# Optimization experiments

Measured on AMD Instinct MI355X. Metric: run time of the kernel, lower is better.

## Reference

```python
import jax, jax.numpy as jnp
import numpy as np

LN_EPS = 1e-5
NORM_EPS = 1e-12  # F.normalize eps


def _l2norm(x):
    # torch F.normalize(p=2, dim=-1): x / max(||x||, eps)
    n = jnp.sqrt(jnp.sum(x * x, axis=-1, keepdims=True))
    return x / jnp.maximum(n, NORM_EPS)


def setup_inputs() -> dict:
    key = jax.random.key(0)
    D, R, H = 256, 32, 64  # d_model, rank, d_model//4
    B, C, P = 32, 64, 96
    ks = jax.random.split(key, 16)
    s = 0.05
    return {
        "x": jax.random.normal(ks[0], (B * C, P, D), jnp.float32),
        "ln_gamma": jnp.ones((D,), jnp.float32),
        "ln_beta": jnp.zeros((D,), jnp.float32),
        "Wd": jax.random.normal(ks[1], (D, R), jnp.float32) * s,
        "bd": jax.random.normal(ks[2], (R,), jnp.float32) * s,
        "Wq": jax.random.normal(ks[3], (R, R), jnp.float32) * s,
        "Wk": jax.random.normal(ks[4], (R, R), jnp.float32) * s,
        "Wv": jax.random.normal(ks[5], (R, R), jnp.float32) * s,
        "Wg": jax.random.normal(ks[6], (R, R), jnp.float32) * s,
        "bg": jax.random.normal(ks[7], (R,), jnp.float32) * s,
        "Wu": jax.random.normal(ks[8], (R, D), jnp.float32) * s,
        "bu": jax.random.normal(ks[9], (D,), jnp.float32) * s,
        "W1": jax.random.normal(ks[10], (D, H), jnp.float32) * s,
        "b1": jax.random.normal(ks[11], (H,), jnp.float32) * s,
        "W2": jax.random.normal(ks[12], (H, D), jnp.float32) * s,
        "b2": jnp.full((D,), -5.0, jnp.float32),  # gate_init bias
        "B": B,
        "C": C,
    }


def reference(x, ln_gamma, ln_beta, Wd, bd, Wq, Wk, Wv, Wg, bg, Wu, bu, W1, b1, W2, b2, B, C):
    BC, P, D = x.shape
    # [B*C, P, D] -> [B*P, C, D] channel-mixing layout
    h = x.reshape(B, C, P, D).transpose(0, 2, 1, 3).reshape(B * P, C, D)

    # LayerNorm over D (biased variance, as in torch LayerNorm)
    mu = jnp.mean(h, axis=-1, keepdims=True)
    var = jnp.var(h, axis=-1, keepdims=True)
    h_norm = (h - mu) * jax.lax.rsqrt(var + LN_EPS) * ln_gamma + ln_beta

    # bottleneck projection to rank R
    h_low = h_norm @ Wd + bd  # [BP, C, R]

    # Hydra linear attention: cosine-normalized Q/K, sum-pooled K*V global feature
    Q = _l2norm(h_low @ Wq)
    K = _l2norm(h_low @ Wk)
    V = h_low @ Wv
    global_feat = jnp.sum(K * V, axis=1, keepdims=True)  # [BP, 1, R]
    h_attn = Q * global_feat

    # content gate and up-projection
    gate_c = jax.nn.sigmoid(h_low @ Wg + bg)
    mixed = (h_attn * gate_c) @ Wu + bu  # [BP, C, D]

    # AdaptiveGate: unbiased variance over channel dim (torch .var default ddof=1)
    chan_var = jnp.var(h, axis=1, ddof=1)  # [BP, D]
    gate_logits = jax.nn.gelu(chan_var @ W1 + b1, approximate=False) @ W2 + b2
    gate = jax.nn.sigmoid(gate_logits)[:, None, :]  # [BP, 1, D]

    out = h + gate * mixed
    # back to [B*C, P, D]
    return out.reshape(B, P, C, D).transpose(0, 2, 1, 3).reshape(BC, P, D)
```

## Files before the change

kernel.cpp:

```cpp
#include <hip/hip_runtime.h>

#define DD 256
#define RR 32
#define CC 64
#define PB 96
#define NT 1024

typedef __attribute__((ext_vector_type(8))) short short8;
typedef __attribute__((ext_vector_type(4))) float f32x4;

__device__ __forceinline__ unsigned short f2b(float f) {
    union { float f; unsigned u; } v; v.f = f;
    unsigned r = v.u + 0x7fffu + ((v.u >> 16) & 1u);
    return (unsigned short)(r >> 16);
}
__device__ __forceinline__ float b2f(unsigned short s) {
    union { unsigned u; float f; } v; v.u = ((unsigned)s) << 16;
    return v.f;
}

__device__ __forceinline__ int hidx(int c, int d) {
    return c * 256 + ((((d >> 3) ^ (c & 7)) << 3) | (d & 7));
}
__device__ __forceinline__ int nidx(int row, int k) {
    return row * 32 + ((((k >> 3) ^ ((row >> 1) & 3)) << 3) | (k & 7));
}

__global__ __launch_bounds__(NT, 8)
void hydra_kernel(const float* __restrict__ x,
                  const float* __restrict__ ln_g, const float* __restrict__ ln_b,
                  const float* __restrict__ Wd, const float* __restrict__ bd,
                  const float* __restrict__ Wq, const float* __restrict__ Wk,
                  const float* __restrict__ Wv, const float* __restrict__ Wg,
                  const float* __restrict__ bg,
                  const float* __restrict__ Wu, const float* __restrict__ bu,
                  const float* __restrict__ W1, const float* __restrict__ b1,
                  const float* __restrict__ W2, const float* __restrict__ b2,
                  float* __restrict__ out)
{
    __shared__ short hbf[CC * DD];
    __shared__ short wreg[RR * DD];
    __shared__ short lowbuf[CC * RR];
    __shared__ short qgkv[2 * CC * RR];
    __shared__ float redA[2048];
    __shared__ float redB[2048];
    __shared__ float mu_s[CC], rstd_s[CC];
    __shared__ float cv_s[DD], gate_s[DD];
    __shared__ float hid_s[64];
    __shared__ float ln_a[RR], ln_bv[RR];

    const int t    = threadIdx.x;
    const int lane = t & 63;
    const int w    = t >> 6;
    const int bp   = blockIdx.x;
    const int b    = bp / PB;
    const int p    = bp - b * PB;
    const size_t rowbase = (size_t)(b * CC) * PB * DD + (size_t)p * DD;

    #pragma unroll
    for (int i = 0; i < 4; ++i) {
        const int c = w * 4 + i;
        const float4 v = *(const float4*)(x + rowbase + (size_t)c * (PB * DD) + 4 * lane);
        float s1 = v.x + v.y + v.z + v.w;
        float s2 = v.x * v.x + v.y * v.y + v.z * v.z + v.w * v.w;
        #pragma unroll
        for (int off = 32; off; off >>= 1) {
            s1 += __shfl_xor(s1, off, 64);
            s2 += __shfl_xor(s2, off, 64);
        }
        if (lane == 0) {
            const float mu = s1 * (1.f / 256.f);
            mu_s[c]   = mu;
            rstd_s[c] = rsqrtf(s2 * (1.f / 256.f) - mu * mu + 1e-5f);
        }
        ushort4 pk;
        pk.x = f2b(v.x); pk.y = f2b(v.y); pk.z = f2b(v.z); pk.w = f2b(v.w);
        *(ushort4*)&hbf[hidx(c, 4 * lane)] = pk;
    }
    {
        const int r = t >> 5, dblk = t & 31;
        short8 vv;
        float sa = 0.f, sb = 0.f;
        #pragma unroll
        for (int j = 0; j < 8; ++j) {
            const int d = dblk * 8 + j;
            const float wd = Wd[d * RR + r];
            const float g  = ln_g[d];
            vv[j] = (short)f2b(g * wd);
            sa += g * wd;
            sb += ln_b[d] * wd;
        }
        *(short8*)&wreg[r * 256 + ((dblk ^ (r & 7)) << 3)] = vv;
        redA[r * 32 + dblk]        = sa;
        redA[1024 + r * 32 + dblk] = sb;
    }
    __syncthreads();

    f32x4 s3acc = {0.f, 0.f, 0.f, 0.f};
    if (w < 8) {
        const int ct = w >> 1, rt = w & 1;
        const int arow = ct * 16 + (lane & 15);
        const int brow = rt * 16 + (lane & 15);
        const int ksub = lane >> 4;
        #pragma unroll
        for (int step = 0; step < 8; ++step) {
            const int kb = step * 4 + ksub;
            const short8 a  = *(const short8*)&hbf[arow * 256 + ((kb ^ (arow & 7)) << 3)];
            const short8 bf = *(const short8*)&wreg[brow * 256 + ((kb ^ (brow & 7)) << 3)];
            s3acc = __builtin_amdgcn_mfma_f32_16x16x32_bf16(a, bf, s3acc, 0, 0, 0);
        }
    } else {
        const int idx = t - 512;
        const int dp  = idx & 127;
        const int rg  = idx >> 7;
        const int d0  = dp * 2;
        float s1a = 0.f, s1b = 0.f, s2a = 0.f, s2b = 0.f;
        #pragma unroll 4
        for (int i = 0; i < 16; ++i) {
            const int c = rg * 16 + i;
            const ushort2 u = *(const ushort2*)&hbf[hidx(c, d0)];
            const float va = b2f(u.x), vb = b2f(u.y);
            s1a += va; s2a += va * va;
            s1b += vb; s2b += vb * vb;
        }
        *(float2*)&redB[rg * 256 + d0]        = make_float2(s1a, s1b);
        *(float2*)&redB[1024 + rg * 256 + d0] = make_float2(s2a, s2b);
        if (idx < 64) {
            const int r = idx & 31, which = idx >> 5;
            float s = 0.f;
            for (int g = 0; g < 32; ++g) s += redA[which * 1024 + r * 32 + g];
            if (which == 0) ln_a[r] = s;
            else            ln_bv[r] = s + bd[r];
        }
    }
    __syncthreads();

    if (w < 8) {
        const int ct = w >> 1, rt = w & 1;
        const int col = rt * 16 + (lane & 15);
        const float la = ln_a[col], lb = ln_bv[col];
        #pragma unroll
        for (int i = 0; i < 4; ++i) {
            const int c = ct * 16 + (lane >> 4) * 4 + i;
            const float rs = rstd_s[c];
            const float hl = rs * s3acc[i] - rs * mu_s[c] * la + lb;
            lowbuf[nidx(c, col)] = (short)f2b(hl);
        }
    } else {
        const int slot = t - 512;
        const int m = slot >> 7, rr2 = (slot >> 2) & 31, kg = slot & 3;
        const float* Wm = (m == 0) ? Wq : (m == 1) ? Wk : (m == 2) ? Wv : Wg;
        short8 vv;
        #pragma unroll
        for (int j = 0; j < 8; ++j)
            vv[j] = (short)f2b(Wm[(kg * 8 + j) * RR + rr2]);
        *(short8*)&wreg[m * 1024 + nidx(rr2, kg * 8)] = vv;
    }
    if (t < 256) {
        const float S1 = redB[t] + redB[256 + t] + redB[512 + t] + redB[768 + t];
        const float S2 = redB[1024 + t] + redB[1280 + t] + redB[1536 + t] + redB[1792 + t];
        cv_s[t] = (S2 - S1 * S1 * (1.f / 64.f)) * (1.f / 63.f);
    }
    __syncthreads();

    if (w < 8) {
        const int ct = w >> 1, pair = w & 1;
        const int mA = pair ? 1 : 0;
        const int mB = pair ? 2 : 3;
        const int arow = ct * 16 + (lane & 15);
        const int ksub = lane >> 4;
        const short8 a = *(const short8*)&lowbuf[arow * 32 + ((ksub ^ ((arow >> 1) & 3)) << 3)];
        f32x4 aA0 = {0,0,0,0}, aA1 = {0,0,0,0}, aB0 = {0,0,0,0}, aB1 = {0,0,0,0};
        {
            const int br0 = (lane & 15), br1 = 16 + (lane & 15);
            const short8 bA0 = *(const short8*)&wreg[mA * 1024 + br0 * 32 + ((ksub ^ ((br0 >> 1) & 3)) << 3)];
            const short8 bA1 = *(const short8*)&wreg[mA * 1024 + br1 * 32 + ((ksub ^ ((br1 >> 1) & 3)) << 3)];
            const short8 bB0 = *(const short8*)&wreg[mB * 1024 + br0 * 32 + ((ksub ^ ((br0 >> 1) & 3)) << 3)];
            const short8 bB1 = *(const short8*)&wreg[mB * 1024 + br1 * 32 + ((ksub ^ ((br1 >> 1) & 3)) << 3)];
            aA0 = __builtin_amdgcn_mfma_f32_16x16x32_bf16(a, bA0, aA0, 0, 0, 0);
            aA1 = __builtin_amdgcn_mfma_f32_16x16x32_bf16(a, bA1, aA1, 0, 0, 0);
            aB0 = __builtin_amdgcn_mfma_f32_16x16x32_bf16(a, bB0, aB0, 0, 0, 0);
            aB1 = __builtin_amdgcn_mfma_f32_16x16x32_bf16(a, bB1, aB1, 0, 0, 0);
        }
        float qs[4];
        #pragma unroll
        for (int i = 0; i < 4; ++i) {
            float ss = aA0[i] * aA0[i] + aA1[i] * aA1[i];
            ss += __shfl_xor(ss, 1, 64);
            ss += __shfl_xor(ss, 2, 64);
            ss += __shfl_xor(ss, 4, 64);
            ss += __shfl_xor(ss, 8, 64);
            qs[i] = 1.f / fmaxf(sqrtf(ss), 1e-12f);
        }
        const int col0 = (lane & 15), col1 = 16 + (lane & 15);
        float bgv0 = 0.f, bgv1 = 0.f;
        if (pair == 0) { bgv0 = bg[col0]; bgv1 = bg[col1]; }
        #pragma unroll
        for (int i = 0; i < 4; ++i) {
            const int c = ct * 16 + (lane >> 4) * 4 + i;
            float b0 = aB0[i], b1v = aB1[i];
            if (pair == 0) {
                b0  = 1.f / (1.f + __expf(-(b0 + bgv0)));
                b1v = 1.f / (1.f + __expf(-(b1v + bgv1)));
            }
            qgkv[pair * 2048 + c * 32 + col0] = (short)f2b(aA0[i] * qs[i] * b0);
            qgkv[pair * 2048 + c * 32 + col1] = (short)f2b(aA1[i] * qs[i] * b1v);
        }
    } else {
        const int idx = t - 512;
        const int j = idx & 63, dg = idx >> 6;
        float s = 0.f;
        #pragma unroll 8
        for (int i = 0; i < 32; ++i) {
            const int d = dg * 32 + i;
            s += cv_s[d] * W1[d * 64 + j];
        }
        redA[dg * 64 + j] = s;
    }
    __syncthreads();

    if (t < 64) {
        float s = b1[t];
        #pragma unroll
        for (int g = 0; g < 8; ++g) s += redA[g * 64 + t];
        hid_s[t] = 0.5f * s * (1.f + erff(s * 0.70710678118654752f));
    }
    if (t >= 256 && t < 512) {
        const int idx = t - 256;
        const int r = idx & 31, g = idx >> 5;
        float s = 0.f;
        #pragma unroll
        for (int i = 0; i < 8; ++i)
            s += b2f((unsigned short)qgkv[2048 + (g * 8 + i) * 32 + r]);
        redA[512 + g * 32 + r] = s;
    }
    {
        const int d = t & 255, kg = t >> 8;
        short8 vv;
        #pragma unroll
        for (int j = 0; j < 8; ++j)
            vv[j] = (short)f2b(Wu[(kg * 8 + j) * DD + d]);
        *(short8*)&wreg[nidx(d, kg * 8)] = vv;
    }
    __syncthreads();

    {
        const int d = t & 255, jg = t >> 8;
        float s = 0.f;
        #pragma unroll
        for (int i = 0; i < 16; ++i) {
            const int j = jg * 16 + i;
            s += hid_s[j] * W2[j * DD + d];
        }
        redB[jg * 256 + d] = s;
    }
    {
        const int r = t & 31, c0 = t >> 5, c1 = (t >> 5) + 32;
        float gf = 0.f;
        #pragma unroll
        for (int g = 0; g < 8; ++g) gf += redA[512 + g * 32 + r];
        lowbuf[nidx(c0, r)] = (short)f2b(b2f((unsigned short)qgkv[c0 * 32 + r]) * gf);
        lowbuf[nidx(c1, r)] = (short)f2b(b2f((unsigned short)qgkv[c1 * 32 + r]) * gf);
    }
    __syncthreads();

    {
        const int ct = w & 3, dg = w >> 2;
        const int arow = ct * 16 + (lane & 15);
        const int ksub = lane >> 4;
        const short8 a = *(const short8*)&lowbuf[arow * 32 + ((ksub ^ ((arow >> 1) & 3)) << 3)];
        #pragma unroll
        for (int j = 0; j < 4; ++j) {
            const int dt = dg * 4 + j;
            const int col = dt * 16 + (lane & 15);
            const short8 bf = *(const short8*)&wreg[col * 32 + ((ksub ^ ((col >> 1) & 3)) << 3)];
            f32x4 acc = {0.f, 0.f, 0.f, 0.f};
            acc = __builtin_amdgcn_mfma_f32_16x16x32_bf16(a, bf, acc, 0, 0, 0);
            #pragma unroll
            for (int i = 0; i < 4; ++i) {
                const int c = ct * 16 + (lane >> 4) * 4 + i;
                hbf[hidx(c, col)] = (short)f2b(acc[i]);
            }
        }
    }
    if (t < 256) {
        const float s = redB[t] + redB[256 + t] + redB[512 + t] + redB[768 + t] + b2[t];
        gate_s[t] = 1.f / (1.f + __expf(-s));
    }
    __syncthreads();

    #pragma unroll
    for (int i = 0; i < 4; ++i) {
        const int c = w * 4 + i;
        const size_t off = rowbase + (size_t)c * (PB * DD) + 4 * lane;
        const float4 xv = *(const float4*)(x + off);
        const ushort4 m = *(const ushort4*)&hbf[hidx(c, 4 * lane)];
        const float4 g4 = *(const float4*)&gate_s[4 * lane];
        const float4 bu4 = *(const float4*)(bu + 4 * lane);
        float4 o;
        o.x = xv.x + g4.x * (b2f(m.x) + bu4.x);
        o.y = xv.y + g4.y * (b2f(m.y) + bu4.y);
        o.z = xv.z + g4.z * (b2f(m.z) + bu4.z);
        o.w = xv.w + g4.w * (b2f(m.w) + bu4.w);
        *(float4*)(out + off) = o;
    }
}

extern "C" void kernel_launch(void* const* d_in, const int* in_sizes, int n_in,
                              void* d_out, int out_size, void* d_ws, size_t ws_size,
                              hipStream_t stream) {
    (void)in_sizes; (void)n_in; (void)out_size; (void)d_ws; (void)ws_size;
    const float* x    = (const float*)d_in[0];
    const float* ln_g = (const float*)d_in[1];
    const float* ln_b = (const float*)d_in[2];
    const float* Wd   = (const float*)d_in[3];
    const float* bd   = (const float*)d_in[4];
    const float* Wq   = (const float*)d_in[5];
    const float* Wk   = (const float*)d_in[6];
    const float* Wv   = (const float*)d_in[7];
    const float* Wg   = (const float*)d_in[8];
    const float* bg   = (const float*)d_in[9];
    const float* Wu   = (const float*)d_in[10];
    const float* bu   = (const float*)d_in[11];
    const float* W1   = (const float*)d_in[12];
    const float* b1   = (const float*)d_in[13];
    const float* W2   = (const float*)d_in[14];
    const float* b2   = (const float*)d_in[15];
    float* out = (float*)d_out;

    hydra_kernel<<<dim3(32 * PB), dim3(NT), 0, stream>>>(
        x, ln_g, ln_b, Wd, bd, Wq, Wk, Wv, Wg, bg, Wu, bu, W1, b1, W2, b2, out);
}
```

Baseline: 166.2 us.

## Precompute bf16 swizzled weights in a prep kernel and shrink shared memory

```diff
diff --git a/kernel.cpp b/kernel.cpp
--- a/kernel.cpp
+++ b/kernel.cpp
@@ -26,23 +26,81 @@
     return row * 32 + ((((k >> 3) ^ ((row >> 1) & 3)) << 3) | (k & 7));
 }
 
+__global__ __launch_bounds__(1024, 1)
+void prep_kernel(const float* __restrict__ ln_g, const float* __restrict__ ln_b,
+                 const float* __restrict__ Wd, const float* __restrict__ bd,
+                 const float* __restrict__ Wq, const float* __restrict__ Wk,
+                 const float* __restrict__ Wv, const float* __restrict__ Wg,
+                 const float* __restrict__ Wu,
+                 short* __restrict__ wsWd, short* __restrict__ wsQKVG,
+                 short* __restrict__ wsWu, float* __restrict__ wsLN)
+{
+    __shared__ float redp[2048];
+    const int t = threadIdx.x;
+    {
+        const int r = t >> 5, dblk = t & 31;
+        short8 vv;
+        float sa = 0.f, sb = 0.f;
+        #pragma unroll
+        for (int j = 0; j < 8; ++j) {
+            const int d = dblk * 8 + j;
+            const float wd = Wd[d * RR + r];
+            const float g  = ln_g[d];
+            vv[j] = (short)f2b(g * wd);
+            sa += g * wd;
+            sb += ln_b[d] * wd;
+        }
+        *(short8*)&wsWd[r * 256 + ((dblk ^ (r & 7)) << 3)] = vv;
+        redp[r * 32 + dblk]        = sa;
+        redp[1024 + r * 32 + dblk] = sb;
+    }
+    if (t < 512) {
+        const int m = t >> 7, rr2 = (t >> 2) & 31, kg = t & 3;
+        const float* Wm = (m == 0) ? Wq : (m == 1) ? Wk : (m == 2) ? Wv : Wg;
+        short8 vv;
+        #pragma unroll
+        for (int j = 0; j < 8; ++j)
+            vv[j] = (short)f2b(Wm[(kg * 8 + j) * RR + rr2]);
+        *(short8*)&wsQKVG[m * 1024 + rr2 * 32 + ((kg ^ ((rr2 >> 1) & 3)) << 3)] = vv;
+    }
+    {
+        const int d = t & 255, kg = t >> 8;
+        short8 vv;
+        #pragma unroll
+        for (int j = 0; j < 8; ++j)
+            vv[j] = (short)f2b(Wu[(kg * 8 + j) * DD + d]);
+        *(short8*)&wsWu[d * 32 + ((kg ^ ((d >> 1) & 3)) << 3)] = vv;
+    }
+    __syncthreads();
+    if (t < 32) {
+        float s = 0.f;
+        #pragma unroll
+        for (int g = 0; g < 32; ++g) s += redp[t * 32 + g];
+        wsLN[t] = s;
+    } else if (t < 64) {
+        const int r = t - 32;
+        float s = 0.f;
+        #pragma unroll
+        for (int g = 0; g < 32; ++g) s += redp[1024 + r * 32 + g];
+        wsLN[t] = s + bd[r];
+    }
+}
+
 __global__ __launch_bounds__(NT, 8)
 void hydra_kernel(const float* __restrict__ x,
-                  const float* __restrict__ ln_g, const float* __restrict__ ln_b,
-                  const float* __restrict__ Wd, const float* __restrict__ bd,
-                  const float* __restrict__ Wq, const float* __restrict__ Wk,
-                  const float* __restrict__ Wv, const float* __restrict__ Wg,
+                  const short* __restrict__ wsWd, const short* __restrict__ wsQKVG,
+                  const short* __restrict__ wsWu, const float* __restrict__ wsLN,
                   const float* __restrict__ bg,
-                  const float* __restrict__ Wu, const float* __restrict__ bu,
+                  const float* __restrict__ bu,
                   const float* __restrict__ W1, const float* __restrict__ b1,
                   const float* __restrict__ W2, const float* __restrict__ b2,
                   float* __restrict__ out)
 {
     __shared__ short hbf[CC * DD];
-    __shared__ short wreg[RR * DD];
+    __shared__ short wreg[RR * DD / 2];
+    __shared__ short qg[CC * RR];
     __shared__ short lowbuf[CC * RR];
-    __shared__ short qgkv[2 * CC * RR];
-    __shared__ float redA[2048];
+    __shared__ float redA[1024];
     __shared__ float redB[2048];
     __shared__ float mu_s[CC], rstd_s[CC];
     __shared__ float cv_s[DD], gate_s[DD];
@@ -77,23 +135,9 @@
         pk.x = f2b(v.x); pk.y = f2b(v.y); pk.z = f2b(v.z); pk.w = f2b(v.w);
         *(ushort4*)&hbf[hidx(c, 4 * lane)] = pk;
     }
-    {
-        const int r = t >> 5, dblk = t & 31;
-        short8 vv;
-        float sa = 0.f, sb = 0.f;
-        #pragma unroll
-        for (int j = 0; j < 8; ++j) {
-            const int d = dblk * 8 + j;
-            const float wd = Wd[d * RR + r];
-            const float g  = ln_g[d];
-            vv[j] = (short)f2b(g * wd);
-            sa += g * wd;
-            sb += ln_b[d] * wd;
-        }
-        *(short8*)&wreg[r * 256 + ((dblk ^ (r & 7)) << 3)] = vv;
-        redA[r * 32 + dblk]        = sa;
-        redA[1024 + r * 32 + dblk] = sb;
-    }
+    *(short8*)&wreg[t * 8] = *(const short8*)&wsWd[t * 8];
+    if (t < 32)              ln_a[t]       = wsLN[t];
+    else if (t < 64)         ln_bv[t - 32] = wsLN[t];
     __syncthreads();
 
     f32x4 s3acc = {0.f, 0.f, 0.f, 0.f};
@@ -125,13 +169,6 @@
         }
         *(float2*)&redB[rg * 256 + d0]        = make_float2(s1a, s1b);
         *(float2*)&redB[1024 + rg * 256 + d0] = make_float2(s2a, s2b);
-        if (idx < 64) {
-            const int r = idx & 31, which = idx >> 5;
-            float s = 0.f;
-            for (int g = 0; g < 32; ++g) s += redA[which * 1024 + r * 32 + g];
-            if (which == 0) ln_a[r] = s;
-            else            ln_bv[r] = s + bd[r];
-        }
     }
     __syncthreads();
 
@@ -147,14 +184,8 @@
             lowbuf[nidx(c, col)] = (short)f2b(hl);
         }
     } else {
-        const int slot = t - 512;
-        const int m = slot >> 7, rr2 = (slot >> 2) & 31, kg = slot & 3;
-        const float* Wm = (m == 0) ? Wq : (m == 1) ? Wk : (m == 2) ? Wv : Wg;
-        short8 vv;
-        #pragma unroll
-        for (int j = 0; j < 8; ++j)
-            vv[j] = (short)f2b(Wm[(kg * 8 + j) * RR + rr2]);
-        *(short8*)&wreg[m * 1024 + nidx(rr2, kg * 8)] = vv;
+        const int idx = t - 512;
+        *(short8*)&wreg[idx * 8] = *(const short8*)&wsQKVG[idx * 8];
     }
     if (t < 256) {
         const float S1 = redB[t] + redB[256 + t] + redB[512 + t] + redB[768 + t];
@@ -193,18 +224,23 @@
             qs[i] = 1.f / fmaxf(sqrtf(ss), 1e-12f);
         }
         const int col0 = (lane & 15), col1 = 16 + (lane & 15);
-        float bgv0 = 0.f, bgv1 = 0.f;
-        if (pair == 0) { bgv0 = bg[col0]; bgv1 = bg[col1]; }
-        #pragma unroll
-        for (int i = 0; i < 4; ++i) {
-            const int c = ct * 16 + (lane >> 4) * 4 + i;
-            float b0 = aB0[i], b1v = aB1[i];
-            if (pair == 0) {
-                b0  = 1.f / (1.f + __expf(-(b0 + bgv0)));
-                b1v = 1.f / (1.f + __expf(-(b1v + bgv1)));
+        if (pair == 0) {
+            const float bgv0 = bg[col0], bgv1 = bg[col1];
+            #pragma unroll
+            for (int i = 0; i < 4; ++i) {
+                const int c = ct * 16 + (lane >> 4) * 4 + i;
+                const float g0 = 1.f / (1.f + __expf(-(aB0[i] + bgv0)));
+                const float g1 = 1.f / (1.f + __expf(-(aB1[i] + bgv1)));
+                qg[c * 32 + col0] = (short)f2b(aA0[i] * qs[i] * g0);
+                qg[c * 32 + col1] = (short)f2b(aA1[i] * qs[i] * g1);
             }
-            qgkv[pair * 2048 + c * 32 + col0] = (short)f2b(aA0[i] * qs[i] * b0);
-            qgkv[pair * 2048 + c * 32 + col1] = (short)f2b(aA1[i] * qs[i] * b1v);
+        } else {
+            #pragma unroll
+            for (int i = 0; i < 4; ++i) {
+                const int c = ct * 16 + (lane >> 4) * 4 + i;
+                redB[c * 32 + col0] = aA0[i] * qs[i] * aB0[i];
+                redB[c * 32 + col1] = aA1[i] * qs[i] * aB1[i];
+            }
         }
     } else {
         const int idx = t - 512;
@@ -231,17 +267,10 @@
         float s = 0.f;
         #pragma unroll
         for (int i = 0; i < 8; ++i)
-            s += b2f((unsigned short)qgkv[2048 + (g * 8 + i) * 32 + r]);
+            s += redB[(g * 8 + i) * 32 + r];
         redA[512 + g * 32 + r] = s;
     }
-    {
-        const int d = t & 255, kg = t >> 8;
-        short8 vv;
-        #pragma unroll
-        for (int j = 0; j < 8; ++j)
-            vv[j] = (short)f2b(Wu[(kg * 8 + j) * DD + d]);
-        *(short8*)&wreg[nidx(d, kg * 8)] = vv;
-    }
+    *(short8*)&wreg[t * 8] = *(const short8*)&wsWu[t * 8];
     __syncthreads();
 
     {
@@ -254,13 +283,13 @@
         }
         redB[jg * 256 + d] = s;
     }
-    {
+    if (t < 256) {
         const int r = t & 31, c0 = t >> 5, c1 = (t >> 5) + 32;
         float gf = 0.f;
         #pragma unroll
         for (int g = 0; g < 8; ++g) gf += redA[512 + g * 32 + r];
-        lowbuf[nidx(c0, r)] = (short)f2b(b2f((unsigned short)qgkv[c0 * 32 + r]) * gf);
-        lowbuf[nidx(c1, r)] = (short)f2b(b2f((unsigned short)qgkv[c1 * 32 + r]) * gf);
+        lowbuf[nidx(c0, r)] = (short)f2b(b2f((unsigned short)qg[c0 * 32 + r]) * gf);
+        lowbuf[nidx(c1, r)] = (short)f2b(b2f((unsigned short)qg[c1 * 32 + r]) * gf);
     }
     __syncthreads();
 
@@ -309,7 +338,7 @@
 extern "C" void kernel_launch(void* const* d_in, const int* in_sizes, int n_in,
                               void* d_out, int out_size, void* d_ws, size_t ws_size,
                               hipStream_t stream) {
-    (void)in_sizes; (void)n_in; (void)out_size; (void)d_ws; (void)ws_size;
+    (void)in_sizes; (void)n_in; (void)out_size; (void)ws_size;
     const float* x    = (const float*)d_in[0];
     const float* ln_g = (const float*)d_in[1];
     const float* ln_b = (const float*)d_in[2];
@@ -328,6 +357,13 @@
     const float* b2   = (const float*)d_in[15];
     float* out = (float*)d_out;
 
+    short* wsWd   = (short*)d_ws;
+    short* wsQKVG = wsWd + 8192;
+    short* wsWu   = wsQKVG + 4096;
+    float* wsLN   = (float*)(wsWd + 20480);
+
+    prep_kernel<<<dim3(1), dim3(1024), 0, stream>>>(
+        ln_g, ln_b, Wd, bd, Wq, Wk, Wv, Wg, Wu, wsWd, wsQKVG, wsWu, wsLN);
     hydra_kernel<<<dim3(32 * PB), dim3(NT), 0, stream>>>(
-        x, ln_g, ln_b, Wd, bd, Wq, Wk, Wv, Wg, bg, Wu, bu, W1, b1, W2, b2, out);
-}
+        x, wsWd, wsQKVG, wsWu, wsLN, bg, bu, W1, b1, W2, b2, out);
+}
```

Result: faster. 139.7 us (-15.9%).
